# Kernel optimization log

Measured on AMD Instinct MI355X. Metric: run time of the kernel, lower is better.

The kernel has to match this reference:

```python
import jax, jax.numpy as jnp
import numpy as np

# Circuit dimensions: B batch, N sum nodes (rows), C child nodes (cols), NSE stored edges.
B, N, C, NSE = 256, 8192, 32768, 524288


def setup_inputs() -> dict:
    key = jax.random.key(0)
    k1, k2, k3, k4 = jax.random.split(key, 4)
    # child log-likelihoods (output of child_layer.log_likelihood_of_nodes), [B, C]
    child_ll = jax.random.normal(k1, (B, C), dtype=jnp.float32) - 2.0
    # BCOO .data of the (unnormalized) log weights, [NSE]
    log_w_data = jax.random.normal(k2, (NSE,), dtype=jnp.float32)
    # BCOO indices[:, 0]: parent sum-node row of each edge. Guarantee every row
    # appears at least once so no node is empty (log(0) avoided), then sort
    # (matching .sort_indices() row-major ordering).
    rows = jnp.sort(jnp.concatenate([
        jnp.arange(N, dtype=jnp.int32),
        jax.random.randint(k3, (NSE - N,), 0, N, dtype=jnp.int32),
    ]))
    # BCOO indices[:, 1]: child node column of each edge
    cols = jax.random.randint(k4, (NSE,), 0, C, dtype=jnp.int32)
    return {"child_ll": child_ll, "log_w_data": log_w_data,
            "rows": rows, "cols": cols, "n_nodes": N}


def reference(child_ll, log_w_data, rows, cols, n_nodes):
    # log normalization constants per node (max-stabilized, as in
    # SparseSumLayer.log_normalization_constants)
    m = log_w_data.max()
    z = m + jnp.log(jax.ops.segment_sum(jnp.exp(log_w_data - m), rows,
                                        num_segments=n_nodes))  # [N]
    # per-edge: exp(log_w + child_ll[col])  (as in log_likelihood_of_nodes_single)
    vals = jnp.exp(log_w_data[None, :] + child_ll[:, cols])        # [B, NSE]
    # row-wise sparse sum (BCOO .sum(1).todense())
    summed = jax.ops.segment_sum(vals.T, rows, num_segments=n_nodes).T  # [B, N]
    # normalized log-likelihood of each sum node
    return jnp.log(summed) - z[None, :]
```

## Files before the change

### kernel.cpp

```cpp
#include <hip/hip_runtime.h>
#include <hip/hip_bf16.h>

#define BB   256
#define NN   8192
#define CC   32768
#define NSE_ 524288
#define GB   32

__device__ __forceinline__ unsigned int f2bf_rne(float f) {
    unsigned int u = __float_as_uint(f);
    return (u + 0x7fffu + ((u >> 16) & 1u)) >> 16;
}

__global__ __launch_bounds__(256) void prep_cw_kernel(
    const float* __restrict__ lw, const int* __restrict__ rows,
    const int* __restrict__ cols, uint2* __restrict__ cw,
    int* __restrict__ rs) {
    int e = blockIdx.x * 256 + threadIdx.x;
    if (e < NSE_) {
        cw[e] = make_uint2((unsigned)cols[e], __float_as_uint(__expf(lw[e])));
        if (e == 0) { rs[0] = 0; rs[NN] = NSE_; }
        else if (rows[e] != rows[e - 1]) rs[rows[e]] = e;
    } else if (e < NSE_ + 64) {
        cw[e] = make_uint2(0u, 0u);
    }
}

__global__ __launch_bounds__(256) void transpose_kernel(
    const float* __restrict__ ll, unsigned int* __restrict__ cet32) {
    int g = blockIdx.x & 7;
    int ct = blockIdx.x >> 3;
    int c0 = ct * 64, b0 = g * GB;
    __shared__ float tile[64][33];
    int t = threadIdx.x;
    int cl = t & 63, bh = t >> 6;
    #pragma unroll
    for (int k = 0; k < 8; ++k) {
        int bl = bh + 4 * k;
        tile[cl][bl] = ll[(size_t)(b0 + bl) * CC + (c0 + cl)];
    }
    __syncthreads();
    size_t baseu = ((size_t)g * CC + c0) * 16;
    #pragma unroll
    for (int k = 0; k < 4; ++k) {
        int u = t + 256 * k;
        int c = u >> 4, b2 = (u & 15) * 2;
        unsigned int lo = f2bf_rne(__expf(tile[c][b2]));
        unsigned int hi = f2bf_rne(__expf(tile[c][b2 + 1]));
        cet32[baseu + u] = lo | (hi << 16);
    }
}

__global__ __launch_bounds__(256) void sum_rows_kernel(
    const uint2* __restrict__ cw, const int* __restrict__ rs,
    const uint4* __restrict__ cet, float* __restrict__ out) {
    __shared__ float lds_out[32][17];
    int g = blockIdx.x & 7;
    int ntile = blockIdx.x >> 3;
    int n0 = ntile * 16;
    int wv = threadIdx.x >> 6;
    int lane = threadIdx.x & 63;
    int grp = lane >> 2;
    int bq = lane & 3;
    const uint4* slice = cet + (size_t)g * CC * 4;

    for (int r = 0; r < 4; ++r) {
        int n = n0 + wv * 4 + r;
        int s = __builtin_amdgcn_readfirstlane(rs[n]);
        int t = __builtin_amdgcn_readfirstlane(rs[n + 1]);
        float acc[8] = {0.f, 0.f, 0.f, 0.f, 0.f, 0.f, 0.f, 0.f};
        float zs = 0.f;
        #pragma unroll 1
        for (int eb = s; eb < t; eb += 64) {
            #pragma unroll
            for (int j = 0; j < 4; ++j) {
                int e = eb + j * 16 + grp;
                uint2 p = cw[e];
                float w = (e < t) ? __uint_as_float(p.y) : 0.f;
                uint4 u = slice[(p.x << 2) | bq];
                acc[0] = fmaf(w, __uint_as_float(u.x << 16),          acc[0]);
                acc[1] = fmaf(w, __uint_as_float(u.x & 0xffff0000u), acc[1]);
                acc[2] = fmaf(w, __uint_as_float(u.y << 16),          acc[2]);
                acc[3] = fmaf(w, __uint_as_float(u.y & 0xffff0000u), acc[3]);
                acc[4] = fmaf(w, __uint_as_float(u.z << 16),          acc[4]);
                acc[5] = fmaf(w, __uint_as_float(u.z & 0xffff0000u), acc[5]);
                acc[6] = fmaf(w, __uint_as_float(u.w << 16),          acc[6]);
                acc[7] = fmaf(w, __uint_as_float(u.w & 0xffff0000u), acc[7]);
                zs += w;
            }
        }
        #pragma unroll
        for (int off = 4; off <= 32; off <<= 1) {
            #pragma unroll
            for (int k = 0; k < 8; ++k) acc[k] += __shfl_xor(acc[k], off);
            zs += __shfl_xor(zs, off);
        }
        if (grp == 0) {
            float lz = __logf(zs);
            #pragma unroll
            for (int k = 0; k < 8; ++k)
                lds_out[bq * 8 + k][wv * 4 + r] = __logf(acc[k]) - lz;
        }
    }
    __syncthreads();
    if (threadIdx.x < 128) {
        int bl = threadIdx.x >> 2, ch = threadIdx.x & 3;
        float4 v = make_float4(lds_out[bl][ch * 4 + 0], lds_out[bl][ch * 4 + 1],
                               lds_out[bl][ch * 4 + 2], lds_out[bl][ch * 4 + 3]);
        *reinterpret_cast<float4*>(
            out + (size_t)(g * GB + bl) * NN + n0 + ch * 4) = v;
    }
}

extern "C" void kernel_launch(void* const* d_in, const int* in_sizes, int n_in,
                              void* d_out, int out_size, void* d_ws, size_t ws_size,
                              hipStream_t stream) {
    const float* child_ll = (const float*)d_in[0];
    const float* log_w    = (const float*)d_in[1];
    const int*   rows     = (const int*)  d_in[2];
    const int*   cols     = (const int*)  d_in[3];
    float* out = (float*)d_out;

    char* ws = (char*)d_ws;
    uint2*        cwp = (uint2*)ws;
    int*          rs  = (int*)(ws + (size_t)6 * 1024 * 1024);
    unsigned int* cet = (unsigned int*)(ws + (size_t)8 * 1024 * 1024);

    prep_cw_kernel<<<(NSE_ + 64 + 255) / 256, 256, 0, stream>>>(
        log_w, rows, cols, cwp, rs);
    transpose_kernel<<<(CC / 64) * 8, 256, 0, stream>>>(child_ll, cet);
    sum_rows_kernel<<<(NN / 16) * 8, 256, 0, stream>>>(
        cwp, rs, (const uint4*)cet, out);
}
```

Baseline: 135.4 us.

## Fuse prep and transpose kernels, vectorize loads, use packed FMA in gather loop

New measurement: 131.9 us. 1.03x faster.

```diff
diff --git a/kernel.cpp b/kernel.cpp
--- a/kernel.cpp
+++ b/kernel.cpp
@@ -6,43 +6,57 @@
 #define CC   32768
 #define NSE_ 524288
 #define GB   32
+#define PREP_BLOCKS ((NSE_ + 64 + 255) / 256)
+#define TP_TILE 128
+#define TP_BLOCKS ((CC / TP_TILE) * 8)
+
+typedef float v2f __attribute__((ext_vector_type(2)));
 
 __device__ __forceinline__ unsigned int f2bf_rne(float f) {
     unsigned int u = __float_as_uint(f);
     return (u + 0x7fffu + ((u >> 16) & 1u)) >> 16;
 }
 
-__global__ __launch_bounds__(256) void prep_cw_kernel(
+__global__ __launch_bounds__(256) void prep_transpose_kernel(
     const float* __restrict__ lw, const int* __restrict__ rows,
-    const int* __restrict__ cols, uint2* __restrict__ cw,
-    int* __restrict__ rs) {
-    int e = blockIdx.x * 256 + threadIdx.x;
-    if (e < NSE_) {
-        cw[e] = make_uint2((unsigned)cols[e], __float_as_uint(__expf(lw[e])));
-        if (e == 0) { rs[0] = 0; rs[NN] = NSE_; }
-        else if (rows[e] != rows[e - 1]) rs[rows[e]] = e;
-    } else if (e < NSE_ + 64) {
-        cw[e] = make_uint2(0u, 0u);
+    const int* __restrict__ cols, const float* __restrict__ ll,
+    uint2* __restrict__ cw, int* __restrict__ rs,
+    unsigned int* __restrict__ cet32) {
+    int bid = blockIdx.x;
+    int t = threadIdx.x;
+    if (bid < PREP_BLOCKS) {
+        int e = bid * 256 + t;
+        if (e < NSE_) {
+            cw[e] = make_uint2((unsigned)cols[e],
+                               __float_as_uint(__expf(lw[e])));
+            if (e == 0) { rs[0] = 0; rs[NN] = NSE_; }
+            else if (rows[e] != rows[e - 1]) rs[rows[e]] = e;
+        } else if (e < NSE_ + 64) {
+            cw[e] = make_uint2(0u, 0u);
+        }
+        return;
     }
-}
-
-__global__ __launch_bounds__(256) void transpose_kernel(
-    const float* __restrict__ ll, unsigned int* __restrict__ cet32) {
-    int g = blockIdx.x & 7;
-    int ct = blockIdx.x >> 3;
-    int c0 = ct * 64, b0 = g * GB;
-    __shared__ float tile[64][33];
-    int t = threadIdx.x;
-    int cl = t & 63, bh = t >> 6;
+    bid -= PREP_BLOCKS;
+    int g = bid & 7;
+    int ct = bid >> 3;
+    int c0 = ct * TP_TILE, b0 = g * GB;
+    __shared__ float tile[TP_TILE][GB + 1];
     #pragma unroll
-    for (int k = 0; k < 8; ++k) {
-        int bl = bh + 4 * k;
-        tile[cl][bl] = ll[(size_t)(b0 + bl) * CC + (c0 + cl)];
+    for (int k = 0; k < 4; ++k) {
+        int idx = t + 256 * k;
+        int bl = idx >> 5;
+        int c4 = idx & 31;
+        const float4 v = *reinterpret_cast<const float4*>(
+            ll + (size_t)(b0 + bl) * CC + c0 + c4 * 4);
+        tile[c4 * 4 + 0][bl] = v.x;
+        tile[c4 * 4 + 1][bl] = v.y;
+        tile[c4 * 4 + 2][bl] = v.z;
+        tile[c4 * 4 + 3][bl] = v.w;
     }
     __syncthreads();
     size_t baseu = ((size_t)g * CC + c0) * 16;
     #pragma unroll
-    for (int k = 0; k < 4; ++k) {
+    for (int k = 0; k < 8; ++k) {
         int u = t + 256 * k;
         int c = u >> 4, b2 = (u & 15) * 2;
         unsigned int lo = f2bf_rne(__expf(tile[c][b2]));
@@ -68,38 +82,73 @@
         int n = n0 + wv * 4 + r;
         int s = __builtin_amdgcn_readfirstlane(rs[n]);
         int t = __builtin_amdgcn_readfirstlane(rs[n + 1]);
-        float acc[8] = {0.f, 0.f, 0.f, 0.f, 0.f, 0.f, 0.f, 0.f};
+        v2f acc[4];
+        acc[0] = 0.f; acc[1] = 0.f; acc[2] = 0.f; acc[3] = 0.f;
         float zs = 0.f;
-        #pragma unroll 1
-        for (int eb = s; eb < t; eb += 64) {
+        int eb = s;
+        for (; eb + 64 <= t; eb += 64) {
+            #pragma unroll
+            for (int j = 0; j < 4; ++j) {
+                uint2 p = cw[eb + j * 16 + grp];
+                float w = __uint_as_float(p.y);
+                uint4 u = slice[(p.x << 2) | bq];
+                v2f w2; w2.x = w; w2.y = w;
+                v2f g0, g1, g2, g3;
+                g0.x = __uint_as_float(u.x << 16);
+                g0.y = __uint_as_float(u.x & 0xffff0000u);
+                g1.x = __uint_as_float(u.y << 16);
+                g1.y = __uint_as_float(u.y & 0xffff0000u);
+                g2.x = __uint_as_float(u.z << 16);
+                g2.y = __uint_as_float(u.z & 0xffff0000u);
+                g3.x = __uint_as_float(u.w << 16);
+                g3.y = __uint_as_float(u.w & 0xffff0000u);
+                acc[0] += w2 * g0;
+                acc[1] += w2 * g1;
+                acc[2] += w2 * g2;
+                acc[3] += w2 * g3;
+                zs += w;
+            }
+        }
+        if (eb < t) {
             #pragma unroll
             for (int j = 0; j < 4; ++j) {
                 int e = eb + j * 16 + grp;
                 uint2 p = cw[e];
                 float w = (e < t) ? __uint_as_float(p.y) : 0.f;
                 uint4 u = slice[(p.x << 2) | bq];
-                acc[0] = fmaf(w, __uint_as_float(u.x << 16),          acc[0]);
-                acc[1] = fmaf(w, __uint_as_float(u.x & 0xffff0000u), acc[1]);
-                acc[2] = fmaf(w, __uint_as_float(u.y << 16),          acc[2]);
-                acc[3] = fmaf(w, __uint_as_float(u.y & 0xffff0000u), acc[3]);
-                acc[4] = fmaf(w, __uint_as_float(u.z << 16),          acc[4]);
-                acc[5] = fmaf(w, __uint_as_float(u.z & 0xffff0000u), acc[5]);
-                acc[6] = fmaf(w, __uint_as_float(u.w << 16),          acc[6]);
-                acc[7] = fmaf(w, __uint_as_float(u.w & 0xffff0000u), acc[7]);
+                v2f w2; w2.x = w; w2.y = w;
+                v2f g0, g1, g2, g3;
+                g0.x = __uint_as_float(u.x << 16);
+                g0.y = __uint_as_float(u.x & 0xffff0000u);
+                g1.x = __uint_as_float(u.y << 16);
+                g1.y = __uint_as_float(u.y & 0xffff0000u);
+                g2.x = __uint_as_float(u.z << 16);
+                g2.y = __uint_as_float(u.z & 0xffff0000u);
+                g3.x = __uint_as_float(u.w << 16);
+                g3.y = __uint_as_float(u.w & 0xffff0000u);
+                acc[0] += w2 * g0;
+                acc[1] += w2 * g1;
+                acc[2] += w2 * g2;
+                acc[3] += w2 * g3;
                 zs += w;
             }
         }
         #pragma unroll
         for (int off = 4; off <= 32; off <<= 1) {
             #pragma unroll
-            for (int k = 0; k < 8; ++k) acc[k] += __shfl_xor(acc[k], off);
+            for (int k = 0; k < 4; ++k) {
+                acc[k].x += __shfl_xor(acc[k].x, off);
+                acc[k].y += __shfl_xor(acc[k].y, off);
+            }
             zs += __shfl_xor(zs, off);
         }
         if (grp == 0) {
             float lz = __logf(zs);
             #pragma unroll
-            for (int k = 0; k < 8; ++k)
-                lds_out[bq * 8 + k][wv * 4 + r] = __logf(acc[k]) - lz;
+            for (int k = 0; k < 4; ++k) {
+                lds_out[bq * 8 + k * 2 + 0][wv * 4 + r] = __logf(acc[k].x) - lz;
+                lds_out[bq * 8 + k * 2 + 1][wv * 4 + r] = __logf(acc[k].y) - lz;
+            }
         }
     }
     __syncthreads();
@@ -126,9 +175,8 @@
     int*          rs  = (int*)(ws + (size_t)6 * 1024 * 1024);
     unsigned int* cet = (unsigned int*)(ws + (size_t)8 * 1024 * 1024);
 
-    prep_cw_kernel<<<(NSE_ + 64 + 255) / 256, 256, 0, stream>>>(
-        log_w, rows, cols, cwp, rs);
-    transpose_kernel<<<(CC / 64) * 8, 256, 0, stream>>>(child_ll, cet);
+    prep_transpose_kernel<<<PREP_BLOCKS + TP_BLOCKS, 256, 0, stream>>>(
+        log_w, rows, cols, child_ll, cwp, rs, cet);
     sum_rows_kernel<<<(NN / 16) * 8, 256, 0, stream>>>(
         cwp, rs, (const uint4*)cet, out);
 }
```
